# Optimization experiments

Hardware: AMD Instinct MI355X
Metric: run time of the kernel (lower is better)

The kernel has to match this reference:

```python
import jax, jax.numpy as jnp
import numpy as np

H, W = 64, 64          # self.shape = (W, H) = (64, 64)
REG_MAX = 16
TOPK = 4

def _dwconv(y, w, b):
    # y: (N, L, C) -> depthwise 3x3 conv on (N, C, H, W) -> (N, L, C)
    N, L, C = y.shape
    img = jnp.transpose(y, (0, 2, 1)).reshape(N, C, H, W)
    out = jax.lax.conv_general_dilated(
        img, w, (1, 1), ((1, 1), (1, 1)),
        dimension_numbers=('NCHW', 'OIHW', 'NCHW'), feature_group_count=C)
    out = out + b[None, :, None, None]
    return jnp.transpose(out.reshape(N, C, H * W), (0, 2, 1))

def _mlp(x, fc1_w, fc1_b, dw1_w, dw1_b, fc2_w, fc2_b, dw2_w, dw2_b, fc3_w, fc3_b):
    h = x @ fc1_w.T + fc1_b
    h = jax.nn.gelu(_dwconv(h, dw1_w, dw1_b), approximate=False)  # torch nn.GELU is exact erf
    h = h @ fc2_w.T + fc2_b
    h = jax.nn.gelu(_dwconv(h, dw2_w, dw2_b), approximate=False)
    return h @ fc3_w.T + fc3_b

def setup_inputs() -> dict:
    key = jax.random.key(0)
    ks = iter(jax.random.split(key, 16))
    d = {}
    d['x'] = jax.random.normal(next(ks), (1, 32, H * W, 256), dtype=jnp.float32)
    for p in ('c_', 'r_'):
        out3 = 1 if p == 'c_' else 4 * (REG_MAX + 1)
        d[p + 'fc1_w'] = 0.02 * jax.random.normal(next(ks), (256, 256), dtype=jnp.float32)
        d[p + 'fc1_b'] = jnp.zeros((256,), jnp.float32)
        d[p + 'dw1_w'] = 0.3 * jax.random.normal(next(ks), (256, 1, 3, 3), dtype=jnp.float32)
        d[p + 'dw1_b'] = jnp.zeros((256,), jnp.float32)
        d[p + 'fc2_w'] = 0.02 * jax.random.normal(next(ks), (256, 256), dtype=jnp.float32)
        d[p + 'fc2_b'] = jnp.zeros((256,), jnp.float32)
        d[p + 'dw2_w'] = 0.3 * jax.random.normal(next(ks), (256, 1, 3, 3), dtype=jnp.float32)
        d[p + 'dw2_b'] = jnp.zeros((256,), jnp.float32)
        d[p + 'fc3_w'] = 0.02 * jax.random.normal(next(ks), (out3, 256), dtype=jnp.float32)
        d[p + 'fc3_b'] = jnp.zeros((out3,), jnp.float32)
    d['rc1_w'] = 0.1 * jax.random.normal(next(ks), (64, 4 * (TOPK + 1)), dtype=jnp.float32)
    d['rc1_b'] = jnp.zeros((64,), jnp.float32)
    d['rc2_w'] = 0.1 * jax.random.normal(next(ks), (1, 64), dtype=jnp.float32)
    d['rc2_b'] = jnp.zeros((1,), jnp.float32)
    return d

def reference(x,
              c_fc1_w, c_fc1_b, c_dw1_w, c_dw1_b, c_fc2_w, c_fc2_b, c_dw2_w, c_dw2_b, c_fc3_w, c_fc3_b,
              r_fc1_w, r_fc1_b, r_dw1_w, r_dw1_b, r_fc2_w, r_fc2_b, r_dw2_w, r_dw2_b, r_fc3_w, r_fc3_b,
              rc1_w, rc1_b, rc2_w, rc2_b):
    xs = x[0]                                   # (N, L, C)
    N = xs.shape[0]
    reg_pred = _mlp(xs, r_fc1_w, r_fc1_b, r_dw1_w, r_dw1_b, r_fc2_w, r_fc2_b,
                    r_dw2_w, r_dw2_b, r_fc3_w, r_fc3_b)  # (N, L, 4*(reg_max+1))
    prob = jax.nn.softmax(
        jnp.transpose(reg_pred, (0, 2, 1)).reshape(N, 4, REG_MAX + 1, H, W), axis=2)
    pt = jnp.transpose(prob, (0, 1, 3, 4, 2))   # (N,4,H,W,reg_max+1)
    topk, _ = jax.lax.top_k(pt, TOPK)           # (N,4,H,W,topk), sorted desc like torch
    stat = jnp.concatenate([topk, topk.mean(axis=-1, keepdims=True)], axis=-1)
    stat = jnp.transpose(stat, (0, 1, 4, 2, 3)).reshape(N, 4 * (TOPK + 1), H, W)
    q = jax.nn.relu(jnp.einsum('nchw,oc->nohw', stat, rc1_w) + rc1_b[None, :, None, None])
    q = jax.nn.sigmoid(jnp.einsum('nchw,oc->nohw', q, rc2_w) + rc2_b[None, :, None, None])
    cls = _mlp(xs, c_fc1_w, c_fc1_b, c_dw1_w, c_dw1_b, c_fc2_w, c_fc2_b,
               c_dw2_w, c_dw2_b, c_fc3_w, c_fc3_b)      # (N, L, 1)
    cls = jax.nn.sigmoid(jnp.transpose(cls, (0, 2, 1)).reshape(N, 1, H, W)) * q
    proj = jnp.arange(REG_MAX + 1, dtype=reg_pred.dtype)  # linspace(0, reg_max, reg_max+1)
    dist = jax.nn.softmax(reg_pred.reshape(-1, REG_MAX + 1), axis=1) @ proj
    boxes = dist.reshape(N, H, W, 4) / REG_MAX
    return cls, boxes, reg_pred.reshape(N, H, W, 4 * (REG_MAX + 1))
```

## Files before the change

### kernel.cpp

```cpp
#include <hip/hip_runtime.h>
#include <hip/hip_bf16.h>

typedef __bf16 bf16x8 __attribute__((ext_vector_type(8)));
typedef float f32x4 __attribute__((ext_vector_type(4)));
typedef float f32x2 __attribute__((ext_vector_type(2)));

__device__ __forceinline__ float bf2f(unsigned short b) {
  unsigned int u = ((unsigned int)b) << 16;
  return __builtin_bit_cast(float, u);
}
__device__ __forceinline__ unsigned short f2bf(float f) {
  unsigned int u = __builtin_bit_cast(unsigned int, f);
  unsigned int r = u + 0x7fffu + ((u >> 16) & 1u);
  return (unsigned short)(r >> 16);
}
__device__ __forceinline__ f32x2 unpack2(unsigned int u) {
  f32x2 r;
  r.x = __builtin_bit_cast(float, u << 16);
  r.y = __builtin_bit_cast(float, u & 0xffff0000u);
  return r;
}

__device__ __forceinline__ void gload16(const void* g, void* l) {
  typedef __attribute__((address_space(1))) const void* gp_t;
  typedef __attribute__((address_space(3))) void* lp_t;
  __builtin_amdgcn_global_load_lds((gp_t)g, (lp_t)l, 16, 0, 0);
}

__device__ __forceinline__ f32x2 gelu2(f32x2 x) {
  f32x2 z = x * 0.70710678118654752440f;
  f32x2 az; az.x = fabsf(z.x); az.y = fabsf(z.y);
  f32x2 t;
  t.x = __builtin_amdgcn_rcpf(__builtin_fmaf(0.3275911f, az.x, 1.0f));
  t.y = __builtin_amdgcn_rcpf(__builtin_fmaf(0.3275911f, az.y, 1.0f));
  f32x2 y = t * (0.254829592f + t * (-0.284496736f + t * (1.421413741f +
            t * (-1.453152027f + t * 1.061405429f))));
  f32x2 zz = z * z;
  f32x2 e; e.x = __expf(-zz.x); e.y = __expf(-zz.y);
  f32x2 ec = y * e;
  f32x2 d = 0.5f - 0.5f * ec;
  f32x2 ph;
  ph.x = 0.5f + __builtin_copysignf(d.x, z.x);
  ph.y = 0.5f + __builtin_copysignf(d.y, z.y);
  return x * ph;
}

__global__ __launch_bounds__(256) void cvt_x(const float* __restrict__ in,
                                             unsigned short* __restrict__ out) {
  long i = ((long)blockIdx.x * 256 + threadIdx.x) * 8;
  float4 a = *(const float4*)(in + i);
  float4 b = *(const float4*)(in + i + 4);
  __align__(16) unsigned short o[8];
  o[0] = f2bf(a.x); o[1] = f2bf(a.y); o[2] = f2bf(a.z); o[3] = f2bf(a.w);
  o[4] = f2bf(b.x); o[5] = f2bf(b.y); o[6] = f2bf(b.z); o[7] = f2bf(b.w);
  *(uint4*)(out + i) = *(uint4*)o;
}

__global__ __launch_bounds__(256) void prep_all(
    const float* __restrict__ c1w, const float* __restrict__ r1w,
    const float* __restrict__ c2w, const float* __restrict__ r2w,
    const float* __restrict__ c3w, const float* __restrict__ r3w, const float* __restrict__ r3b,
    const float* __restrict__ c1b, const float* __restrict__ r1b,
    const float* __restrict__ c2b, const float* __restrict__ r2b,
    const float* __restrict__ d1wc, const float* __restrict__ d1bc,
    const float* __restrict__ d1wr, const float* __restrict__ d1br,
    const float* __restrict__ d2wc, const float* __restrict__ d2bc,
    const float* __restrict__ d2wr, const float* __restrict__ d2br,
    unsigned short* __restrict__ w1cat, unsigned short* __restrict__ w2cat,
    unsigned short* __restrict__ c3wb, unsigned short* __restrict__ wr3pad,
    float* __restrict__ br3pad, float* __restrict__ b1cat, float* __restrict__ b2cat,
    float* __restrict__ wd1, float* __restrict__ bd1,
    float* __restrict__ wd2, float* __restrict__ bd2) {
  int i = blockIdx.x * 256 + threadIdx.x;
  {
    int which = i >> 16, j = i & 65535;
    float v = (which == 0) ? c1w[j] : (which == 1) ? r1w[j] : (which == 2) ? c2w[j] : r2w[j];
    unsigned short* dst = (which < 2) ? (w1cat + which * 65536) : (w2cat + (which - 2) * 65536);
    dst[j] = f2bf(v);
  }
  if (i < 32768) {
    int r = i >> 8, c = i & 255;
    wr3pad[i] = (r < 68) ? f2bf(r3w[r * 256 + c]) : (unsigned short)0;
    if (i < 128) br3pad[i] = (i < 68) ? r3b[i] : 0.f;
  }
  if (i < 256) c3wb[i] = f2bf(c3w[i]);
  if (i < 4608) {
    int tap = i >> 9, ch = i & 511, cc = ch & 255;
    wd1[i] = (ch < 256) ? d1wc[cc * 9 + tap] : d1wr[cc * 9 + tap];
    wd2[i] = (ch < 256) ? d2wc[cc * 9 + tap] : d2wr[cc * 9 + tap];
  }
  if (i < 512) {
    bd1[i] = (i < 256) ? d1bc[i] : d1br[i & 255];
    bd2[i] = (i < 256) ? d2bc[i] : d2br[i & 255];
    b1cat[i] = (i < 256) ? c1b[i] : r1b[i & 255];
    b2cat[i] = (i < 256) ? c2b[i] : r2b[i & 255];
  }
}

__global__ __launch_bounds__(256, 3) void gemm_glds(
    const unsigned short* __restrict__ A, int lda, int zAoff,
    const unsigned short* __restrict__ W, int zWoff,
    const float* __restrict__ bias, int zBoff,
    unsigned short* __restrict__ Out, int ldo, int zOoff, int lnN) {
  __shared__ unsigned short lds[2][8192];
  const int z = blockIdx.z;
  const unsigned short* Az = A + (long)z * zAoff;
  const unsigned short* Wz = W + (long)z * zWoff;
  const float* biasz = bias + z * zBoff;
  unsigned short* Outz = Out + (long)z * zOoff;

  const int nwg = gridDim.x;
  const int bid = blockIdx.x;
  const int wg = (bid & 7) * (nwg >> 3) + (bid >> 3);
  const int mtile = wg >> lnN;
  const int ntile = wg & ((1 << lnN) - 1);
  const long row0 = (long)mtile * 128;
  const int col0 = ntile * 128;

  const int tid = threadIdx.x;
  const int lane = tid & 63;
  const int wid = tid >> 6;
  const int wr = (wid >> 1) * 64;
  const int wc = (wid & 1) * 64;
  const int rr = lane & 15;
  const int gk = lane >> 4;
  const int swz = (rr >> 1) & 3;

  const int srow_l = (wid << 4) + (lane >> 2);
  const int sgl = lane & 3;

  f32x4 acc[4][4] = {};

  auto stage = [&](int buf, int k0) {
    #pragma unroll
    for (int j = 0; j < 4; j++) {
      const int slotbase = j * 256 + (wid << 6);
      unsigned short* ldst = &lds[buf][slotbase * 8];
      const int row = (j & 1) * 64 + srow_l;
      const int g = sgl ^ ((row >> 1) & 3);
      const unsigned short* src;
      if (j < 2) src = Az + (row0 + row) * (long)lda + k0 + g * 8;
      else       src = Wz + (long)(col0 + row) * 256 + k0 + g * 8;
      gload16(src, ldst);
    }
  };

  stage(0, 0);
  #pragma unroll
  for (int ks = 0; ks < 8; ks++) {
    if (ks < 7) {
      stage((ks + 1) & 1, (ks + 1) * 32);
      asm volatile("s_waitcnt vmcnt(4)" ::: "memory");
    } else {
      asm volatile("s_waitcnt vmcnt(0)" ::: "memory");
    }
    __builtin_amdgcn_s_barrier();
    asm volatile("" ::: "memory");
    const unsigned short* buf = lds[ks & 1];
    bf16x8 af[4], bf[4];
    #pragma unroll
    for (int mi = 0; mi < 4; mi++)
      af[mi] = __builtin_bit_cast(bf16x8,
          *(const uint4*)&buf[(wr + mi * 16 + rr) * 32 + ((gk ^ swz) * 8)]);
    #pragma unroll
    for (int ni = 0; ni < 4; ni++)
      bf[ni] = __builtin_bit_cast(bf16x8,
          *(const uint4*)&buf[4096 + (wc + ni * 16 + rr) * 32 + ((gk ^ swz) * 8)]);
    #pragma unroll
    for (int mi = 0; mi < 4; mi++)
      #pragma unroll
      for (int ni = 0; ni < 4; ni++)
        acc[mi][ni] = __builtin_amdgcn_mfma_f32_16x16x32_bf16(af[mi], bf[ni], acc[mi][ni], 0, 0, 0);
    asm volatile("" ::: "memory");
    __builtin_amdgcn_s_barrier();
  }

  #pragma unroll
  for (int mi = 0; mi < 4; mi++) {
    const int rbase = wr + mi * 16 + (lane >> 4) * 4;
    #pragma unroll
    for (int ni = 0; ni < 4; ni++) {
      const int c_ = wc + ni * 16 + (lane & 15);
      const float bv = biasz[col0 + c_];
      #pragma unroll
      for (int r = 0; r < 4; r++) {
        Outz[(row0 + rbase + r) * (long)ldo + col0 + c_] = f2bf(acc[mi][ni][r] + bv);
      }
    }
  }
}

__global__ __launch_bounds__(256) void dwconv_gelu4(
    const unsigned short* __restrict__ In,
    const float* __restrict__ Wt, const float* __restrict__ Bt,
    unsigned short* __restrict__ Out) {
  const int t = blockIdx.x * 256 + threadIdx.x;
  const int g = t & 63;
  const int p = t >> 6;
  const int n = p >> 10;
  const int h = (p >> 4) & 63;
  const int w0 = (p & 15) << 2;
  const int cbase = g << 3;
  f32x2 acc[4][4];
  {
    float4 b0 = *(const float4*)(Bt + cbase);
    float4 b1 = *(const float4*)(Bt + cbase + 4);
    f32x2 bb[4];
    bb[0].x = b0.x; bb[0].y = b0.y; bb[1].x = b0.z; bb[1].y = b0.w;
    bb[2].x = b1.x; bb[2].y = b1.y; bb[3].x = b1.z; bb[3].y = b1.w;
    #pragma unroll
    for (int k = 0; k < 4; k++)
      #pragma unroll
      for (int i = 0; i < 4; i++) acc[k][i] = bb[i];
  }
  #pragma unroll
  for (int dy = -1; dy <= 1; dy++) {
    const int hh = h + dy;
    if (hh < 0 || hh > 63) continue;
    const float* wbase = Wt + ((dy + 1) * 3) * 512 + cbase;
    f32x2 wt[3][4];
    #pragma unroll
    for (int j = 0; j < 3; j++) {
      float4 a0 = *(const float4*)(wbase + j * 512);
      float4 a1 = *(const float4*)(wbase + j * 512 + 4);
      wt[j][0].x = a0.x; wt[j][0].y = a0.y; wt[j][1].x = a0.z; wt[j][1].y = a0.w;
      wt[j][2].x = a1.x; wt[j][2].y = a1.y; wt[j][3].x = a1.z; wt[j][3].y = a1.w;
    }
    const long rowtok = (long)(((n << 6) + hh) << 6);
    f32x2 f[6][4];
    #pragma unroll
    for (int d = 0; d < 6; d++) {
      const int col = w0 - 1 + d;
      uint4 v = {0u, 0u, 0u, 0u};
      if (col >= 0 && col < 64)
        v = *(const uint4*)(In + (rowtok + col) * 512 + cbase);
      f[d][0] = unpack2(v.x); f[d][1] = unpack2(v.y);
      f[d][2] = unpack2(v.z); f[d][3] = unpack2(v.w);
    }
    #pragma unroll
    for (int k = 0; k < 4; k++)
      #pragma unroll
      for (int j = 0; j < 3; j++)
        #pragma unroll
        for (int i = 0; i < 4; i++)
          acc[k][i] += f[k + j][i] * wt[j][i];
  }
  const long mbase = ((long)((n << 6) + h) << 6) + w0;
  #pragma unroll
  for (int k = 0; k < 4; k++) {
    __align__(16) unsigned short ov[8];
    #pragma unroll
    for (int i = 0; i < 4; i++) {
      f32x2 ge = gelu2(acc[k][i]);
      ov[2 * i] = f2bf(ge.x); ov[2 * i + 1] = f2bf(ge.y);
    }
    *(uint4*)(Out + (mbase + k) * 512 + cbase) = *(uint4*)ov;
  }
}

__global__ __launch_bounds__(256) void cls_dot(
    const unsigned short* __restrict__ G2,
    const unsigned short* __restrict__ Wc3,
    const float* __restrict__ bc3,
    float* __restrict__ cls_logit) {
  int lane = threadIdx.x & 63;
  int wid = threadIdx.x >> 6;
  long m = (long)blockIdx.x * 4 + wid;
  const unsigned short* row = G2 + m * 512;
  ushort4 a = *(const ushort4*)(row + lane * 4);
  ushort4 wv = *(const ushort4*)(Wc3 + lane * 4);
  float s = bf2f(a.x) * bf2f(wv.x) + bf2f(a.y) * bf2f(wv.y) +
            bf2f(a.z) * bf2f(wv.z) + bf2f(a.w) * bf2f(wv.w);
  #pragma unroll
  for (int off = 32; off > 0; off >>= 1) s += __shfl_down(s, off);
  if (lane == 0) cls_logit[m] = s + bc3[0];
}

__global__ __launch_bounds__(256) void post_kernel(
    const unsigned short* __restrict__ RP,
    const float* __restrict__ cls_logit,
    const float* __restrict__ rc1_w, const float* __restrict__ rc1_b,
    const float* __restrict__ rc2_w, const float* __restrict__ rc2_b,
    float* __restrict__ out_cls, float* __restrict__ out_boxes, float* __restrict__ out_reg) {
  int m = blockIdx.x * 256 + threadIdx.x;
  const unsigned short* rp = RP + (long)m * 128;
  float stat[20];
  #pragma unroll
  for (int s = 0; s < 4; s++) {
    float v[17];
    float mx = -1e30f;
    #pragma unroll
    for (int i = 0; i < 17; i++) {
      v[i] = bf2f(rp[s * 17 + i]);
      out_reg[(long)m * 68 + s * 17 + i] = v[i];
      mx = fmaxf(mx, v[i]);
    }
    float sum = 0.f;
    #pragma unroll
    for (int i = 0; i < 17; i++) { v[i] = __expf(v[i] - mx); sum += v[i]; }
    float inv = 1.f / sum;
    float dist = 0.f;
    #pragma unroll
    for (int i = 0; i < 17; i++) { v[i] *= inv; dist += v[i] * (float)i; }
    out_boxes[(long)m * 4 + s] = dist * 0.0625f;
    float tk[4];
    #pragma unroll
    for (int t = 0; t < 4; t++) {
      float bm = v[0]; int bi = 0;
      #pragma unroll
      for (int i = 1; i < 17; i++) {
        if (v[i] > bm) { bm = v[i]; bi = i; }
      }
      tk[t] = bm;
      #pragma unroll
      for (int i = 0; i < 17; i++)
        if (i == bi) v[i] = -1.f;
    }
    stat[s * 5 + 0] = tk[0]; stat[s * 5 + 1] = tk[1];
    stat[s * 5 + 2] = tk[2]; stat[s * 5 + 3] = tk[3];
    stat[s * 5 + 4] = 0.25f * (tk[0] + tk[1] + tk[2] + tk[3]);
  }
  float z = 0.f;
  #pragma unroll
  for (int o = 0; o < 64; o++) {
    float q = rc1_b[o];
    #pragma unroll
    for (int c = 0; c < 20; c++) q += rc1_w[o * 20 + c] * stat[c];
    q = fmaxf(q, 0.f);
    z += q * rc2_w[o];
  }
  z += rc2_b[0];
  float q2 = 1.f / (1.f + __expf(-z));
  float cl = 1.f / (1.f + __expf(-cls_logit[m]));
  out_cls[m] = cl * q2;
}

extern "C" void kernel_launch(void* const* d_in, const int* in_sizes, int n_in,
                              void* d_out, int out_size, void* d_ws, size_t ws_size,
                              hipStream_t stream) {
  const float* x       = (const float*)d_in[0];
  const float* c_fc1_w = (const float*)d_in[1];
  const float* c_fc1_b = (const float*)d_in[2];
  const float* c_dw1_w = (const float*)d_in[3];
  const float* c_dw1_b = (const float*)d_in[4];
  const float* c_fc2_w = (const float*)d_in[5];
  const float* c_fc2_b = (const float*)d_in[6];
  const float* c_dw2_w = (const float*)d_in[7];
  const float* c_dw2_b = (const float*)d_in[8];
  const float* c_fc3_w = (const float*)d_in[9];
  const float* c_fc3_b = (const float*)d_in[10];
  const float* r_fc1_w = (const float*)d_in[11];
  const float* r_fc1_b = (const float*)d_in[12];
  const float* r_dw1_w = (const float*)d_in[13];
  const float* r_dw1_b = (const float*)d_in[14];
  const float* r_fc2_w = (const float*)d_in[15];
  const float* r_fc2_b = (const float*)d_in[16];
  const float* r_dw2_w = (const float*)d_in[17];
  const float* r_dw2_b = (const float*)d_in[18];
  const float* r_fc3_w = (const float*)d_in[19];
  const float* r_fc3_b = (const float*)d_in[20];
  const float* rc1_w   = (const float*)d_in[21];
  const float* rc1_b   = (const float*)d_in[22];
  const float* rc2_w   = (const float*)d_in[23];
  const float* rc2_b   = (const float*)d_in[24];

  char* ws = (char*)d_ws;
  unsigned short* Hbuf = (unsigned short*)ws;
  unsigned short* Gbuf = (unsigned short*)(ws + 134217728L);
  unsigned short* xb   = Gbuf;
  unsigned short* RP   = (unsigned short*)(ws + 268435456L);
  float* cls_logit     = (float*)(ws + 301989888L);
  char* wb             = ws + 302514176L;
  unsigned short* w1cat  = (unsigned short*)wb;
  unsigned short* w2cat  = w1cat + 131072;
  unsigned short* c3wb   = w2cat + 131072;
  unsigned short* wr3pad = c3wb + 256;
  float* br3pad = (float*)(wr3pad + 32768);
  float* b1cat  = br3pad + 128;
  float* b2cat  = b1cat + 512;
  float* wd1    = b2cat + 512;
  float* bd1    = wd1 + 4608;
  float* wd2    = bd1 + 512;
  float* bd2    = wd2 + 4608;

  prep_all<<<1024, 256, 0, stream>>>(
      c_fc1_w, r_fc1_w, c_fc2_w, r_fc2_w, c_fc3_w, r_fc3_w, r_fc3_b,
      c_fc1_b, r_fc1_b, c_fc2_b, r_fc2_b,
      c_dw1_w, c_dw1_b, r_dw1_w, r_dw1_b,
      c_dw2_w, c_dw2_b, r_dw2_w, r_dw2_b,
      w1cat, w2cat, c3wb, wr3pad, br3pad, b1cat, b2cat,
      wd1, bd1, wd2, bd2);
  cvt_x<<<16384, 256, 0, stream>>>(x, xb);

  gemm_glds<<<dim3(4096, 1, 1), 256, 0, stream>>>(
      xb, 256, 0, w1cat, 0, b1cat, 0, Hbuf, 512, 0, 2);
  dwconv_gelu4<<<8192, 256, 0, stream>>>(Hbuf, wd1, bd1, Gbuf);
  gemm_glds<<<dim3(2048, 1, 2), 256, 0, stream>>>(
      Gbuf, 512, 256, w2cat, 65536, b2cat, 256, Hbuf, 512, 256, 1);
  dwconv_gelu4<<<8192, 256, 0, stream>>>(Hbuf, wd2, bd2, Gbuf);
  cls_dot<<<32768, 256, 0, stream>>>(Gbuf, c3wb, c_fc3_b, cls_logit);
  gemm_glds<<<dim3(1024, 1, 1), 256, 0, stream>>>(
      Gbuf + 256, 512, 0, wr3pad, 0, br3pad, 0, RP, 128, 0, 0);
  float* out_cls   = (float*)d_out;
  float* out_boxes = out_cls + 131072;
  float* out_reg   = out_boxes + 524288;
  post_kernel<<<512, 256, 0, stream>>>(RP, cls_logit, rc1_w, rc1_b, rc2_w, rc2_b,
                                       out_cls, out_boxes, out_reg);
}
```

Before: 378.4 us.

## Triple-buffer GEMM LDS pipeline and fuse cls dot product into second dwconv

The GEMM main loop moves from double to triple buffering in LDS, issuing loads three K-steps ahead and refilling a buffer after its compute barrier. The separate cls_dot kernel is removed, and the second dwconv+GELU kernel now computes the cls fc3 dot product in registers with a shuffle reduction. That kernel also skips writing the cls-half channels, which nothing reads. This cuts one launch and a full re-read of the cls activations, at the cost of 48KB of LDS per GEMM block, which may lower occupancy against the launch bound of 3.

```diff
diff --git a/kernel.cpp b/kernel.cpp
--- a/kernel.cpp
+++ b/kernel.cpp
@@ -102,7 +102,7 @@
     const unsigned short* __restrict__ W, int zWoff,
     const float* __restrict__ bias, int zBoff,
     unsigned short* __restrict__ Out, int ldo, int zOoff, int lnN) {
-  __shared__ unsigned short lds[2][8192];
+  __shared__ unsigned short lds[3][8192];
   const int z = blockIdx.z;
   const unsigned short* Az = A + (long)z * zAoff;
   const unsigned short* Wz = W + (long)z * zWoff;
@@ -146,17 +146,16 @@
   };
 
   stage(0, 0);
+  stage(1, 32);
+  stage(2, 64);
   #pragma unroll
   for (int ks = 0; ks < 8; ks++) {
-    if (ks < 7) {
-      stage((ks + 1) & 1, (ks + 1) * 32);
-      asm volatile("s_waitcnt vmcnt(4)" ::: "memory");
-    } else {
-      asm volatile("s_waitcnt vmcnt(0)" ::: "memory");
-    }
+    if (ks <= 5)      asm volatile("s_waitcnt vmcnt(8)" ::: "memory");
+    else if (ks == 6) asm volatile("s_waitcnt vmcnt(4)" ::: "memory");
+    else              asm volatile("s_waitcnt vmcnt(0)" ::: "memory");
     __builtin_amdgcn_s_barrier();
     asm volatile("" ::: "memory");
-    const unsigned short* buf = lds[ks & 1];
+    const unsigned short* buf = lds[ks % 3];
     bf16x8 af[4], bf[4];
     #pragma unroll
     for (int mi = 0; mi < 4; mi++)
@@ -173,6 +172,7 @@
         acc[mi][ni] = __builtin_amdgcn_mfma_f32_16x16x32_bf16(af[mi], bf[ni], acc[mi][ni], 0, 0, 0);
     asm volatile("" ::: "memory");
     __builtin_amdgcn_s_barrier();
+    if (ks <= 4) stage((ks + 3) % 3, (ks + 3) * 32);
   }
 
   #pragma unroll
@@ -190,10 +190,13 @@
   }
 }
 
+template <bool CLS>
 __global__ __launch_bounds__(256) void dwconv_gelu4(
     const unsigned short* __restrict__ In,
     const float* __restrict__ Wt, const float* __restrict__ Bt,
-    unsigned short* __restrict__ Out) {
+    unsigned short* __restrict__ Out,
+    const unsigned short* __restrict__ Wc3, const float* __restrict__ bc3,
+    float* __restrict__ cls_logit) {
   const int t = blockIdx.x * 256 + threadIdx.x;
   const int g = t & 63;
   const int p = t >> 6;
@@ -245,35 +248,44 @@
         for (int i = 0; i < 4; i++)
           acc[k][i] += f[k + j][i] * wt[j][i];
   }
+  f32x2 w3[4];
+  if (CLS) {
+    const int cc = cbase & 255;
+    uint4 wv = *(const uint4*)(Wc3 + cc);
+    w3[0] = unpack2(wv.x); w3[1] = unpack2(wv.y);
+    w3[2] = unpack2(wv.z); w3[3] = unpack2(wv.w);
+  }
   const long mbase = ((long)((n << 6) + h) << 6) + w0;
+  float s[4];
   #pragma unroll
   for (int k = 0; k < 4; k++) {
     __align__(16) unsigned short ov[8];
+    f32x2 ge[4];
     #pragma unroll
     for (int i = 0; i < 4; i++) {
-      f32x2 ge = gelu2(acc[k][i]);
-      ov[2 * i] = f2bf(ge.x); ov[2 * i + 1] = f2bf(ge.y);
-    }
-    *(uint4*)(Out + (mbase + k) * 512 + cbase) = *(uint4*)ov;
-  }
-}
-
-__global__ __launch_bounds__(256) void cls_dot(
-    const unsigned short* __restrict__ G2,
-    const unsigned short* __restrict__ Wc3,
-    const float* __restrict__ bc3,
-    float* __restrict__ cls_logit) {
-  int lane = threadIdx.x & 63;
-  int wid = threadIdx.x >> 6;
-  long m = (long)blockIdx.x * 4 + wid;
-  const unsigned short* row = G2 + m * 512;
-  ushort4 a = *(const ushort4*)(row + lane * 4);
-  ushort4 wv = *(const ushort4*)(Wc3 + lane * 4);
-  float s = bf2f(a.x) * bf2f(wv.x) + bf2f(a.y) * bf2f(wv.y) +
-            bf2f(a.z) * bf2f(wv.z) + bf2f(a.w) * bf2f(wv.w);
-  #pragma unroll
-  for (int off = 32; off > 0; off >>= 1) s += __shfl_down(s, off);
-  if (lane == 0) cls_logit[m] = s + bc3[0];
+      ge[i] = gelu2(acc[k][i]);
+      ov[2 * i] = f2bf(ge[i].x); ov[2 * i + 1] = f2bf(ge[i].y);
+    }
+    if (!CLS || cbase >= 256)
+      *(uint4*)(Out + (mbase + k) * 512 + cbase) = *(uint4*)ov;
+    if (CLS) {
+      f32x2 sp = ge[0] * w3[0] + ge[1] * w3[1] + ge[2] * w3[2] + ge[3] * w3[3];
+      s[k] = sp.x + sp.y;
+    }
+  }
+  if (CLS) {
+    #pragma unroll
+    for (int k = 0; k < 4; k++) {
+      #pragma unroll
+      for (int m = 16; m >= 1; m >>= 1) s[k] += __shfl_xor(s[k], m);
+    }
+    if (g == 0) {
+      float b = bc3[0];
+      float4 o;
+      o.x = s[0] + b; o.y = s[1] + b; o.z = s[2] + b; o.w = s[3] + b;
+      *(float4*)(cls_logit + mbase) = o;
+    }
+  }
 }
 
 __global__ __launch_bounds__(256) void post_kernel(
@@ -394,11 +406,12 @@
 
   gemm_glds<<<dim3(4096, 1, 1), 256, 0, stream>>>(
       xb, 256, 0, w1cat, 0, b1cat, 0, Hbuf, 512, 0, 2);
-  dwconv_gelu4<<<8192, 256, 0, stream>>>(Hbuf, wd1, bd1, Gbuf);
+  dwconv_gelu4<false><<<8192, 256, 0, stream>>>(Hbuf, wd1, bd1, Gbuf,
+                                                nullptr, nullptr, nullptr);
   gemm_glds<<<dim3(2048, 1, 2), 256, 0, stream>>>(
       Gbuf, 512, 256, w2cat, 65536, b2cat, 256, Hbuf, 512, 256, 1);
-  dwconv_gelu4<<<8192, 256, 0, stream>>>(Hbuf, wd2, bd2, Gbuf);
-  cls_dot<<<32768, 256, 0, stream>>>(Gbuf, c3wb, c_fc3_b, cls_logit);
+  dwconv_gelu4<true><<<8192, 256, 0, stream>>>(Hbuf, wd2, bd2, Gbuf,
+                                               c3wb, c_fc3_b, cls_logit);
   gemm_glds<<<dim3(1024, 1, 1), 256, 0, stream>>>(
       Gbuf + 256, 512, 0, wr3pad, 0, br3pad, 0, RP, 128, 0, 0);
   float* out_cls   = (float*)d_out;
```

New measurement: 360.3 us. 1.05x faster.
